# Performance work log

Measured on AMD Instinct MI355X. Metric: run time of the kernel, lower is better.

## Reference

```python
import jax, jax.numpy as jnp
import numpy as np

B, N, C = 4, 2048, 1024
H = 8
D = C // H  # head dim = 128
SCALE = D ** -0.5
EPS = 1e-5


def setup_inputs() -> dict:
    key = jax.random.key(0)
    ks = jax.random.split(key, 12)
    s = 0.02
    return {
        "x": jax.random.normal(ks[0], (B, N, C), jnp.float32),
        "ln1_g": jnp.ones((C,), jnp.float32),
        "ln1_b": jnp.zeros((C,), jnp.float32),
        "w_qkv": jax.random.normal(ks[1], (3 * C, C), jnp.float32) * s,  # torch Linear weight [out,in], no bias
        "w_proj": jax.random.normal(ks[2], (C, C), jnp.float32) * s,
        "b_proj": jnp.zeros((C,), jnp.float32),
        "ln2_g": jnp.ones((C,), jnp.float32),
        "ln2_b": jnp.zeros((C,), jnp.float32),
        "w1": jax.random.normal(ks[3], (C, C), jnp.float32) * s,
        "b1": jnp.full((C,), 0.1, jnp.float32),
        "w2": jax.random.normal(ks[4], (C, C), jnp.float32) * s,
        "b2": jnp.full((C,), 0.1, jnp.float32),
        "bn_g": jnp.ones((C,), jnp.float32),
        "bn_b": jnp.zeros((C,), jnp.float32),
        "bn_mean": jnp.zeros((C,), jnp.float32),
        "bn_var": jnp.ones((C,), jnp.float32),
    }


def _layernorm(x, g, b):
    mu = jnp.mean(x, axis=-1, keepdims=True)
    var = jnp.mean(jnp.square(x - mu), axis=-1, keepdims=True)
    return (x - mu) * jax.lax.rsqrt(var + EPS) * g + b


def reference(x, ln1_g, ln1_b, w_qkv, w_proj, b_proj, ln2_g, ln2_b,
              w1, b1, w2, b2, bn_g, bn_b, bn_mean, bn_var):
    # --- attention branch (pre-LN) ---
    h = _layernorm(x, ln1_g, ln1_b)
    qkv = h @ w_qkv.T                              # [B,N,3C]
    qkv = qkv.reshape(B, N, 3, H, D)
    q = qkv[:, :, 0].transpose(0, 2, 1, 3)         # [B,H,N,D]
    k = qkv[:, :, 1].transpose(0, 2, 1, 3)
    v = qkv[:, :, 2].transpose(0, 2, 1, 3)
    attn = jnp.einsum('bhnd,bhmd->bhnm', q, k) * SCALE
    attn = jax.nn.softmax(attn, axis=-1)
    o = jnp.einsum('bhnm,bhmd->bhnd', attn, v)     # [B,H,N,D]
    o = o.transpose(0, 2, 1, 3).reshape(B, N, C)
    x = x + (o @ w_proj.T + b_proj)

    # --- MLP branch (pre-LN), ELU + eval-mode BatchNorm ---
    h = _layernorm(x, ln2_g, ln2_b)
    h = jax.nn.elu(h @ w1.T + b1)
    h = jax.nn.elu(h @ w2.T + b2)
    h = (h - bn_mean) * jax.lax.rsqrt(bn_var + EPS) * bn_g + bn_b
    return x + h
```

## Files before the change

kernel.cpp:

```cpp
#include <hip/hip_runtime.h>
#include <hip/hip_bf16.h>

using u16 = unsigned short;
typedef __attribute__((ext_vector_type(8))) __bf16 bf16x8;
typedef __attribute__((ext_vector_type(4))) float f32x4;
typedef __attribute__((ext_vector_type(16))) float f32x16;
typedef __attribute__((ext_vector_type(4))) unsigned int u32x4;
typedef __attribute__((ext_vector_type(2))) unsigned int u32x2;

#define LN_EPS 1e-5f
#define ATT_SCALE 0.08838834764831845f

__device__ __forceinline__ u16 f2bf(float f) {
    unsigned int u = __builtin_bit_cast(unsigned int, f);
    u += 0x7FFFu + ((u >> 16) & 1u);
    return (u16)(u >> 16);
}

__device__ __forceinline__ bf16x8 ld_frag(const u16* p) {
    return __builtin_bit_cast(bf16x8, *(const u32x4*)p);
}

__device__ __forceinline__ unsigned pack_bf2(float lo, float hi) {
    return __builtin_amdgcn_perm(__builtin_bit_cast(unsigned, hi),
                                 __builtin_bit_cast(unsigned, lo), 0x07060302u);
}

__device__ __forceinline__ void gl_lds(const u16* g, u16* l) {
    __builtin_amdgcn_global_load_lds((const __attribute__((address_space(1))) void*)g,
                                     (__attribute__((address_space(3))) void*)l, 16, 0, 0);
}

__global__ __launch_bounds__(256)
void cvt_ln(const float* __restrict__ x, const float* __restrict__ g,
            const float* __restrict__ b, u16* __restrict__ hout,
            const float* __restrict__ w_qkv, const float* __restrict__ w_proj,
            const float* __restrict__ w1, const float* __restrict__ w2,
            u16* __restrict__ wout)
{
    const int t = threadIdx.x;
    if (blockIdx.x < 8192) {
        const int row = blockIdx.x;
        const float4 v = ((const float4*)(x + (size_t)row * 1024))[t];
        float s  = v.x + v.y + v.z + v.w;
        float ss = v.x * v.x + v.y * v.y + v.z * v.z + v.w * v.w;
        #pragma unroll
        for (int d = 32; d > 0; d >>= 1) { s += __shfl_down(s, d); ss += __shfl_down(ss, d); }
        __shared__ float red[8];
        const int wave = t >> 6, lane = t & 63;
        if (lane == 0) { red[wave] = s; red[4 + wave] = ss; }
        __syncthreads();
        const float S  = red[0] + red[1] + red[2] + red[3];
        const float SS = red[4] + red[5] + red[6] + red[7];
        const float mu = S * (1.f / 1024.f);
        const float rstd = rsqrtf(SS * (1.f / 1024.f) - mu * mu + LN_EPS);
        const float4 gv = ((const float4*)g)[t];
        const float4 bv = ((const float4*)b)[t];
        ushort4 ov;
        ov.x = f2bf((v.x - mu) * rstd * gv.x + bv.x);
        ov.y = f2bf((v.y - mu) * rstd * gv.y + bv.y);
        ov.z = f2bf((v.z - mu) * rstd * gv.z + bv.z);
        ov.w = f2bf((v.w - mu) * rstd * gv.w + bv.w);
        ((ushort4*)(hout + (size_t)row * 1024))[t] = ov;
    } else {
        const int i = (blockIdx.x - 8192) * 256 + t;
        const int n_qkv = 3072 * 1024 / 4, n_c = 1024 * 1024 / 4;
        const float* src;
        int j = i;
        if (j < n_qkv) { src = w_qkv; }
        else if ((j -= n_qkv) < n_c) { src = w_proj; }
        else if ((j -= n_c) < n_c)   { src = w1; }
        else { j -= n_c; src = w2; }
        const float4 v = ((const float4*)src)[j];
        ushort4 o;
        o.x = f2bf(v.x); o.y = f2bf(v.y); o.z = f2bf(v.z); o.w = f2bf(v.w);
        ((ushort4*)wout)[i] = o;
    }
}

__global__ __launch_bounds__(256)
void ln_kernel(const float* __restrict__ x, const float* __restrict__ g,
               const float* __restrict__ b, u16* __restrict__ out)
{
    const int row = blockIdx.x;
    const int t = threadIdx.x;
    const float4 v = ((const float4*)(x + (size_t)row * 1024))[t];
    float s  = v.x + v.y + v.z + v.w;
    float ss = v.x * v.x + v.y * v.y + v.z * v.z + v.w * v.w;
    #pragma unroll
    for (int d = 32; d > 0; d >>= 1) { s += __shfl_down(s, d); ss += __shfl_down(ss, d); }
    __shared__ float red[8];
    const int wave = t >> 6, lane = t & 63;
    if (lane == 0) { red[wave] = s; red[4 + wave] = ss; }
    __syncthreads();
    const float S  = red[0] + red[1] + red[2] + red[3];
    const float SS = red[4] + red[5] + red[6] + red[7];
    const float mu = S * (1.f / 1024.f);
    const float rstd = rsqrtf(SS * (1.f / 1024.f) - mu * mu + LN_EPS);
    const float4 gv = ((const float4*)g)[t];
    const float4 bv = ((const float4*)b)[t];
    ushort4 ov;
    ov.x = f2bf((v.x - mu) * rstd * gv.x + bv.x);
    ov.y = f2bf((v.y - mu) * rstd * gv.y + bv.y);
    ov.z = f2bf((v.z - mu) * rstd * gv.z + bv.z);
    ov.w = f2bf((v.w - mu) * rstd * gv.w + bv.w);
    ((ushort4*)(out + (size_t)row * 1024))[t] = ov;
}

#define WAITVM12 { asm volatile("s_waitcnt vmcnt(12)" ::: "memory"); __builtin_amdgcn_sched_barrier(0); }
#define WAITVM8  { asm volatile("s_waitcnt vmcnt(8)"  ::: "memory"); __builtin_amdgcn_sched_barrier(0); }
#define WAITVM4  { asm volatile("s_waitcnt vmcnt(4)"  ::: "memory"); __builtin_amdgcn_sched_barrier(0); }
#define WAITVM0  { asm volatile("s_waitcnt vmcnt(0)"  ::: "memory"); __builtin_amdgcn_sched_barrier(0); }

#define GEMM_PREAMBLE(Aptr, Bptr, Kdim)                                           \
    __shared__ __align__(16) u16 As[4][128 * 32];                                 \
    __shared__ __align__(16) u16 Bs[4][128 * 32];                                 \
    const int tid  = threadIdx.x;                                                 \
    const int wave = tid >> 6;                                                    \
    const int lane = tid & 63;                                                    \
    const int quad = lane >> 4;                                                   \
    const int l16  = lane & 15;                                                   \
    const int m0 = blockIdx.x * 128;                                              \
    const int n0 = blockIdx.y * 128;                                              \
    const int wm = (wave & 1) * 64;                                               \
    const int wn = (wave >> 1) * 64;                                              \
    f32x4 acc[4][4];                                                              \
    _Pragma("unroll")                                                             \
    for (int i = 0; i < 4; i++)                                                   \
        _Pragma("unroll")                                                         \
        for (int j = 0; j < 4; j++)                                               \
            acc[i][j] = f32x4{0.f, 0.f, 0.f, 0.f};                                \
    \
    \
    const u16* gA = Aptr + (size_t)(m0 + (tid >> 2)) * Kdim                       \
                    + (((tid & 3) ^ ((tid >> 3) & 3)) * 8);                       \
    const u16* gB = Bptr + (size_t)(n0 + (tid >> 2)) * Kdim                       \
                    + (((tid & 3) ^ ((tid >> 3) & 3)) * 8);                       \
    auto STAGE = [&](int kt, int bf) {                                            \
        _Pragma("unroll")                                                         \
        for (int rnd = 0; rnd < 2; rnd++) {                                       \
            gl_lds(gA + (size_t)rnd * 64 * Kdim + kt * 32,                        \
                   &As[bf][rnd * 2048 + wave * 512]);                             \
            gl_lds(gB + (size_t)rnd * 64 * Kdim + kt * 32,                        \
                   &Bs[bf][rnd * 2048 + wave * 512]);                             \
        }                                                                         \
    };                                                                            \
    const int NT = Kdim / 32;                                                     \
    STAGE(0, 0); STAGE(1, 1); STAGE(2, 2);                                        \
    for (int t = 0; t < NT; t++) {                                                \
        __builtin_amdgcn_sched_barrier(0);                                        \
        __builtin_amdgcn_s_barrier();         \
        __builtin_amdgcn_sched_barrier(0);                                        \
        if (t + 3 < NT) STAGE(t + 3, (t + 3) & 3);                                \
        if (t < NT - 3)       WAITVM12                                            \
        else if (t == NT - 3) WAITVM8                                             \
        else if (t == NT - 2) WAITVM4                                             \
        else                  WAITVM0                                             \
        __builtin_amdgcn_s_barrier();        \
        __builtin_amdgcn_sched_barrier(0);                                        \
        const u16* curA = As[t & 3];                                              \
        const u16* curB = Bs[t & 3];                                              \
        bf16x8 af[4], bfv[4];                                                     \
        _Pragma("unroll")                                                         \
        for (int i = 0; i < 4; i++) {                                             \
            const int row = wm + i * 16 + l16;                                    \
            const int c = quad ^ ((row >> 1) & 3);                                \
            af[i] = ld_frag(&curA[row * 32 + c * 8]);                             \
        }                                                                         \
        _Pragma("unroll")                                                         \
        for (int j = 0; j < 4; j++) {                                             \
            const int row = wn + j * 16 + l16;                                    \
            const int c = quad ^ ((row >> 1) & 3);                                \
            bfv[j] = ld_frag(&curB[row * 32 + c * 8]);                            \
        }                                                                         \
        __builtin_amdgcn_s_setprio(1);                                            \
        _Pragma("unroll")                                                         \
        for (int i = 0; i < 4; i++)                                               \
            _Pragma("unroll")                                                     \
            for (int j = 0; j < 4; j++)                                           \
                acc[i][j] = __builtin_amdgcn_mfma_f32_16x16x32_bf16(              \
                    af[i], bfv[j], acc[i][j], 0, 0, 0);                           \
        __builtin_amdgcn_s_setprio(0);                                            \
    }

__global__ __launch_bounds__(256, 2)
void gemm_qkv(const u16* __restrict__ A, const u16* __restrict__ Bw,
              u16* __restrict__ Cb, u16* __restrict__ Cv)
{
    GEMM_PREAMBLE(A, Bw, 1024)

    #pragma unroll
    for (int j = 0; j < 4; j++) {
        const int gn = n0 + wn + j * 16 + l16;
        if (gn < 2048) {
            const float qs = (gn < 1024) ? ATT_SCALE : 1.0f;
            #pragma unroll
            for (int i = 0; i < 4; i++) {
                const int gm0 = m0 + wm + i * 16 + quad * 4;
                #pragma unroll
                for (int r = 0; r < 4; r++)
                    Cb[(size_t)(gm0 + r) * 2048 + gn] = f2bf(acc[i][j][r] * qs);
            }
        } else {
            const int hh = (gn >> 7) & 7, dd = gn & 127;
            #pragma unroll
            for (int i = 0; i < 4; i++) {
                const int gm0 = m0 + wm + i * 16 + quad * 4;
                #pragma unroll
                for (int r = 0; r < 4; r++) {
                    const int tok = gm0 + r;
                    Cv[((size_t)((tok >> 11) * 8 + hh) * 128 + dd) * 2048 + (tok & 2047)] =
                        f2bf(acc[i][j][r]);
                }
            }
        }
    }
}

template <int EPI>
__global__ __launch_bounds__(256, 2)
void gemm_c(const u16* __restrict__ A, const u16* __restrict__ Bw,
            const float* __restrict__ bias, const float* __restrict__ res,
            float* __restrict__ Cf, u16* __restrict__ Cb,
            const float* __restrict__ bng, const float* __restrict__ bnb,
            const float* __restrict__ bnm, const float* __restrict__ bnv)
{
    const int N = 1024;
    GEMM_PREAMBLE(A, Bw, 1024)

    #pragma unroll
    for (int j = 0; j < 4; j++) {
        const int gn = n0 + wn + j * 16 + l16;
        float bs = bias[gn], sc = 0.f, sh = 0.f;
        if constexpr (EPI == 3) {
            const float iv = rsqrtf(bnv[gn] + LN_EPS);
            sc = bng[gn] * iv;
            sh = bnb[gn] - bnm[gn] * sc;
        }
        #pragma unroll
        for (int i = 0; i < 4; i++) {
            const int gm0 = m0 + wm + i * 16 + quad * 4;
            #pragma unroll
            for (int r = 0; r < 4; r++) {
                const size_t idx = (size_t)(gm0 + r) * N + gn;
                const float v = acc[i][j][r];
                if constexpr (EPI == 1) {
                    Cf[idx] = res[idx] + v + bs;
                } else if constexpr (EPI == 2) {
                    float t = v + bs;
                    t = t > 0.f ? t : (__expf(t) - 1.f);
                    Cb[idx] = f2bf(t);
                } else {
                    float t = v + bs;
                    t = t > 0.f ? t : (__expf(t) - 1.f);
                    t = t * sc + sh;
                    Cf[idx] = res[idx] + t;
                }
            }
        }
    }
}

__global__ __launch_bounds__(256, 2)
void attn_kernel(const u16* __restrict__ qk, const u16* __restrict__ vT, u16* __restrict__ o)
{
    __shared__ __align__(16) u16 smem[32768];

    const int tid  = threadIdx.x;
    const int wave = tid >> 6;
    const int lane = tid & 63;
    const int l32  = lane & 31;
    const int hl   = lane >> 5;
    const int id   = blockIdx.x;
    const int bh   = ((id >> 7) << 3) | (id & 7);
    const int qt   = (id >> 3) & 15;
    const int b    = bh >> 3, h = bh & 7;
    const size_t tok0 = (size_t)b * 2048;

    const u16* qptr = qk + h * 128;
    const u16* kptr = qk + 1024 + h * 128;
    const u16* vptr = vT + (size_t)bh * 128 * 2048;

    #pragma unroll
    for (int qq = 0; qq < 8; qq++) {
        const int s = qq * 256 + tid;
        const int r = s >> 4;
        const int cg = (s & 15) ^ (r & 7);
        const u16* g = qptr + (tok0 + qt * 128 + r) * 2048 + cg * 8;
        const int sb = 16384 + (qq * 256 + (tid & 192)) * 8;
        gl_lds(g, smem + sb);
    }
    __syncthreads();

    bf16x8 qf[8];
    {
        const int row = wave * 32 + l32;
        #pragma unroll
        for (int ks = 0; ks < 8; ks++) {
            const int c = (ks * 2 + hl) ^ (row & 7);
            qf[ks] = ld_frag(smem + 16384 + row * 128 + c * 8);
        }
    }

    f32x16 oacc[4];
    #pragma unroll
    for (int i = 0; i < 4; i++)
        #pragma unroll
        for (int e = 0; e < 16; e++) oacc[i][e] = 0.f;
    float l_acc = 0.f;

    {
        #pragma unroll
        for (int qq = 0; qq < 4; qq++) {
            const int s = qq * 256 + tid;
            const int rk = s >> 4, ck = (s & 15) ^ (rk & 7);
            gl_lds(kptr + (tok0 + rk) * 2048 + ck * 8,
                   smem + (qq * 256 + (tid & 192)) * 8);
            const int rv = s >> 3, cv = (s & 7) ^ (rv & 7);
            gl_lds(vptr + (size_t)rv * 2048 + cv * 8,
                   smem + 8192 + (qq * 256 + (tid & 192)) * 8);
        }
    }

    for (int kt = 0; kt < 32; kt++) {
        __syncthreads();

        if (kt + 1 < 32) {
            u16* nb = smem + ((kt + 1) & 1) * 16384;
            #pragma unroll
            for (int qq = 0; qq < 4; qq++) {
                const int s = qq * 256 + tid;
                const int rk = s >> 4, ck = (s & 15) ^ (rk & 7);
                gl_lds(kptr + (tok0 + (kt + 1) * 64 + rk) * 2048 + ck * 8,
                       nb + (qq * 256 + (tid & 192)) * 8);
                const int rv = s >> 3, cv = (s & 7) ^ (rv & 7);
                gl_lds(vptr + (size_t)rv * 2048 + (kt + 1) * 64 + cv * 8,
                       nb + 8192 + (qq * 256 + (tid & 192)) * 8);
            }
        }

        const u16* Ks = smem + (kt & 1) * 16384;
        const u16* Vs = Ks + 8192;

        f32x16 sacc[2];
        #pragma unroll
        for (int t = 0; t < 2; t++)
            #pragma unroll
            for (int e = 0; e < 16; e++) sacc[t][e] = 0.f;
        __builtin_amdgcn_s_setprio(1);
        #pragma unroll
        for (int ks = 0; ks < 8; ks++) {
            #pragma unroll
            for (int mt = 0; mt < 2; mt++) {
                const int row = mt * 32 + l32;
                const int c = (ks * 2 + hl) ^ (row & 7);
                const bf16x8 kf = ld_frag(Ks + row * 128 + c * 8);
                sacc[mt] = __builtin_amdgcn_mfma_f32_32x32x16_bf16(kf, qf[ks], sacc[mt], 0, 0, 0);
            }
        }
        __builtin_amdgcn_s_setprio(0);

        unsigned pk[2][8];
        #pragma unroll
        for (int t = 0; t < 2; t++) {
            #pragma unroll
            for (int r2 = 0; r2 < 8; r2++) {
                const float p0 = __expf(sacc[t][2 * r2]);
                const float p1 = __expf(sacc[t][2 * r2 + 1]);
                l_acc += p0 + p1;
                pk[t][r2] = pack_bf2(p0, p1);
            }
        }

        #pragma unroll
        for (int ks = 0; ks < 4; ks++) {
            const int t = ks >> 1;
            const int pb = (ks & 1) * 4;
            const u32x2 r02 = __builtin_amdgcn_permlane32_swap(pk[t][pb + 0], pk[t][pb + 2], false, false);
            const u32x2 r13 = __builtin_amdgcn_permlane32_swap(pk[t][pb + 1], pk[t][pb + 3], false, false);
            u32x4 pu;
            pu.x = r02.x; pu.y = r13.x; pu.z = r02.y; pu.w = r13.y;
            const bf16x8 pf = __builtin_bit_cast(bf16x8, pu);
            __builtin_amdgcn_s_setprio(1);
            #pragma unroll
            for (int dt = 0; dt < 4; dt++) {
                const int row = dt * 32 + l32;
                const int c = (ks * 2 + hl) ^ (row & 7);
                const bf16x8 vf = ld_frag(Vs + row * 64 + c * 8);
                oacc[dt] = __builtin_amdgcn_mfma_f32_32x32x16_bf16(vf, pf, oacc[dt], 0, 0, 0);
            }
            __builtin_amdgcn_s_setprio(0);
        }
    }

    __syncthreads();
    u16* Ot = smem;
    const float lt  = l_acc + __shfl_xor(l_acc, 32);
    const float inv = 1.0f / lt;
    const int qloc = wave * 32 + l32;
    #pragma unroll
    for (int dt = 0; dt < 4; dt++) {
        #pragma unroll
        for (int r2 = 0; r2 < 8; r2++) {
            const float v0 = oacc[dt][2 * r2] * inv;
            const float v1 = oacc[dt][2 * r2 + 1] * inv;
            const int dp = dt * 32 + 4 * hl + 2 * (r2 & 1) + 8 * (r2 >> 1);
            *(unsigned*)(Ot + qloc * 136 + dp) = pack_bf2(v0, v1);
        }
    }
    __syncthreads();
    const int qr = tid >> 1;
    const int hh = tid & 1;
    const u16* src = Ot + qr * 136 + hh * 64;
    u16* dst = o + (tok0 + qt * 128 + qr) * 1024 + h * 128 + hh * 64;
    #pragma unroll
    for (int c = 0; c < 8; c++)
        *(u32x4*)(dst + c * 8) = *(const u32x4*)(src + c * 8);
}

extern "C" void kernel_launch(void* const* d_in, const int* in_sizes, int n_in,
                              void* d_out, int out_size, void* d_ws, size_t ws_size,
                              hipStream_t stream)
{
    const float* x      = (const float*)d_in[0];
    const float* ln1_g  = (const float*)d_in[1];
    const float* ln1_b  = (const float*)d_in[2];
    const float* w_qkv  = (const float*)d_in[3];
    const float* w_proj = (const float*)d_in[4];
    const float* b_proj = (const float*)d_in[5];
    const float* ln2_g  = (const float*)d_in[6];
    const float* ln2_b  = (const float*)d_in[7];
    const float* w1     = (const float*)d_in[8];
    const float* b1     = (const float*)d_in[9];
    const float* w2     = (const float*)d_in[10];
    const float* b2     = (const float*)d_in[11];
    const float* bn_g   = (const float*)d_in[12];
    const float* bn_b   = (const float*)d_in[13];
    const float* bn_m   = (const float*)d_in[14];
    const float* bn_v   = (const float*)d_in[15];
    float* out = (float*)d_out;

    u16* wq   = (u16*)d_ws;
    u16* wp   = wq  + (size_t)3072 * 1024;
    u16* w1b  = wp  + (size_t)1024 * 1024;
    u16* w2b  = w1b + (size_t)1024 * 1024;
    u16* hbuf = w2b + (size_t)1024 * 1024;
    u16* qkb  = hbuf + (size_t)8192 * 1024;
    u16* vTb  = qkb + (size_t)8192 * 2048;
    u16* obuf = vTb + (size_t)8192 * 1024;
    float* x1 = (float*)(obuf + (size_t)8192 * 1024);

    cvt_ln<<<14336, 256, 0, stream>>>(x, ln1_g, ln1_b, hbuf, w_qkv, w_proj, w1, w2, wq);

    gemm_qkv<<<dim3(64, 24), 256, 0, stream>>>(hbuf, wq, qkb, vTb);

    attn_kernel<<<512, 256, 0, stream>>>(qkb, vTb, obuf);

    gemm_c<1><<<dim3(64, 8), 256, 0, stream>>>(obuf, wp,
        b_proj, x, x1, nullptr, nullptr, nullptr, nullptr, nullptr);

    ln_kernel<<<8192, 256, 0, stream>>>(x1, ln2_g, ln2_b, hbuf);

    gemm_c<2><<<dim3(64, 8), 256, 0, stream>>>(hbuf, w1b,
        b1, nullptr, nullptr, obuf, nullptr, nullptr, nullptr, nullptr);

    gemm_c<3><<<dim3(64, 8), 256, 0, stream>>>(obuf, w2b,
        b2, x1, out, nullptr, bn_g, bn_b, bn_m, bn_v);
}
```

Baseline: 382.6 us.

## Replace 4-stage GEMM LDS pipeline with double buffering and raise occupancy

Shrinks the GEMM shared-memory staging from four buffers to two and replaces the hand-tuned vmcnt waits and split barriers with one __syncthreads per K-step. The smaller LDS footprint lets the launch bounds ask for three blocks per CU instead of two, so more waves can hide latency. In exchange, the prefetch distance drops from three tiles to one. The full vmcnt(0) drain at each barrier may leave the MFMA units waiting on global loads.

```diff
diff --git a/kernel.cpp b/kernel.cpp
--- a/kernel.cpp
+++ b/kernel.cpp
@@ -107,14 +107,9 @@
     ((ushort4*)(out + (size_t)row * 1024))[t] = ov;
 }
 
-#define WAITVM12 { asm volatile("s_waitcnt vmcnt(12)" ::: "memory"); __builtin_amdgcn_sched_barrier(0); }
-#define WAITVM8  { asm volatile("s_waitcnt vmcnt(8)"  ::: "memory"); __builtin_amdgcn_sched_barrier(0); }
-#define WAITVM4  { asm volatile("s_waitcnt vmcnt(4)"  ::: "memory"); __builtin_amdgcn_sched_barrier(0); }
-#define WAITVM0  { asm volatile("s_waitcnt vmcnt(0)"  ::: "memory"); __builtin_amdgcn_sched_barrier(0); }
-
 #define GEMM_PREAMBLE(Aptr, Bptr, Kdim)                                           \
-    __shared__ __align__(16) u16 As[4][128 * 32];                                 \
-    __shared__ __align__(16) u16 Bs[4][128 * 32];                                 \
+    __shared__ __align__(16) u16 As[2][128 * 32];                                 \
+    __shared__ __align__(16) u16 Bs[2][128 * 32];                                 \
     const int tid  = threadIdx.x;                                                 \
     const int wave = tid >> 6;                                                    \
     const int lane = tid & 63;                                                    \
@@ -132,34 +127,30 @@
             acc[i][j] = f32x4{0.f, 0.f, 0.f, 0.f};                                \
     \
     \
-    const u16* gA = Aptr + (size_t)(m0 + (tid >> 2)) * Kdim                       \
-                    + (((tid & 3) ^ ((tid >> 3) & 3)) * 8);                       \
-    const u16* gB = Bptr + (size_t)(n0 + (tid >> 2)) * Kdim                       \
-                    + (((tid & 3) ^ ((tid >> 3) & 3)) * 8);                       \
-    auto STAGE = [&](int kt, int bf) {                                            \
-        _Pragma("unroll")                                                         \
-        for (int rnd = 0; rnd < 2; rnd++) {                                       \
-            gl_lds(gA + (size_t)rnd * 64 * Kdim + kt * 32,                        \
-                   &As[bf][rnd * 2048 + wave * 512]);                             \
-            gl_lds(gB + (size_t)rnd * 64 * Kdim + kt * 32,                        \
-                   &Bs[bf][rnd * 2048 + wave * 512]);                             \
+    const int srow = tid >> 2;                                                    \
+    const int scol = ((tid & 3) ^ ((tid >> 3) & 3)) * 8;                          \
+    const u16* gA = Aptr + (size_t)(m0 + srow) * Kdim + scol;                     \
+    const u16* gB = Bptr + (size_t)(n0 + srow) * Kdim + scol;                     \
+    const int NT = Kdim / 32;                                                     \
+                                               \
+    _Pragma("unroll")                                                             \
+    for (int rnd = 0; rnd < 2; rnd++) {                                           \
+        gl_lds(gA + (size_t)rnd * 64 * Kdim, &As[0][rnd * 2048 + wave * 512]);    \
+        gl_lds(gB + (size_t)rnd * 64 * Kdim, &Bs[0][rnd * 2048 + wave * 512]);    \
+    }                                                                             \
+    for (int t = 0; t < NT; t++) {                                                \
+        __syncthreads();  \
+        if (t + 1 < NT) {                                                         \
+            u16* dA = &As[(t + 1) & 1][wave * 512];                               \
+            u16* dB = &Bs[(t + 1) & 1][wave * 512];                               \
+            _Pragma("unroll")                                                     \
+            for (int rnd = 0; rnd < 2; rnd++) {                                   \
+                gl_lds(gA + (size_t)rnd * 64 * Kdim + (t + 1) * 32, dA + rnd * 2048); \
+                gl_lds(gB + (size_t)rnd * 64 * Kdim + (t + 1) * 32, dB + rnd * 2048); \
+            }                                                                     \
         }                                                                         \
-    };                                                                            \
-    const int NT = Kdim / 32;                                                     \
-    STAGE(0, 0); STAGE(1, 1); STAGE(2, 2);                                        \
-    for (int t = 0; t < NT; t++) {                                                \
-        __builtin_amdgcn_sched_barrier(0);                                        \
-        __builtin_amdgcn_s_barrier();         \
-        __builtin_amdgcn_sched_barrier(0);                                        \
-        if (t + 3 < NT) STAGE(t + 3, (t + 3) & 3);                                \
-        if (t < NT - 3)       WAITVM12                                            \
-        else if (t == NT - 3) WAITVM8                                             \
-        else if (t == NT - 2) WAITVM4                                             \
-        else                  WAITVM0                                             \
-        __builtin_amdgcn_s_barrier();        \
-        __builtin_amdgcn_sched_barrier(0);                                        \
-        const u16* curA = As[t & 3];                                              \
-        const u16* curB = Bs[t & 3];                                              \
+        const u16* curA = As[t & 1];                                              \
+        const u16* curB = Bs[t & 1];                                              \
         bf16x8 af[4], bfv[4];                                                     \
         _Pragma("unroll")                                                         \
         for (int i = 0; i < 4; i++) {                                             \
@@ -183,7 +174,7 @@
         __builtin_amdgcn_s_setprio(0);                                            \
     }
 
-__global__ __launch_bounds__(256, 2)
+__global__ __launch_bounds__(256, 3)
 void gemm_qkv(const u16* __restrict__ A, const u16* __restrict__ Bw,
               u16* __restrict__ Cb, u16* __restrict__ Cv)
 {
@@ -218,7 +209,7 @@
 }
 
 template <int EPI>
-__global__ __launch_bounds__(256, 2)
+__global__ __launch_bounds__(256, 3)
 void gemm_c(const u16* __restrict__ A, const u16* __restrict__ Bw,
             const float* __restrict__ bias, const float* __restrict__ res,
             float* __restrict__ Cf, u16* __restrict__ Cb,
```

New measurement: 391.5 us. 1.02x slower.
